# Performance work log

Hardware: AMD Instinct MI355X
Metric: run time of the kernel (lower is better)

Reference implementation:

```python
import jax, jax.numpy as jnp
import numpy as np

N_NODES = 30000
N_EDGES = 480000
N_GRAPHS = 10
NODES_PER_GRAPH = 3000
MAX_RADIUS = 4.0
NUM_BASIS = 10
NUM_NEIGHBORS = 16
DIMS = [8, 288, 288, 288, 3]


def _spherical_harmonics(u):
    """e3nn-style real SH, lmax=2, 'component' normalization, on unit vectors u [E,3]."""
    x, y, z = u[:, 0], u[:, 1], u[:, 2]
    s3, s5, s15 = 3.0 ** 0.5, 5.0 ** 0.5, 15.0 ** 0.5
    return jnp.stack([
        jnp.ones_like(x),                      # l=0
        s3 * x, s3 * y, s3 * z,                # l=1
        s15 * x * z,                           # l=2
        s15 * x * y,
        s5 * (y * y - 0.5 * (x * x + z * z)),
        s15 * y * z,
        (s15 / 2.0) * (z * z - x * x),
    ], axis=1)  # [E, 9]


def _soft_one_hot_smooth_finite(r):
    """soft_one_hot_linspace(r, 0, MAX_RADIUS, NUM_BASIS, 'smooth_finite', cutoff=True)."""
    values = jnp.linspace(0.0, MAX_RADIUS, NUM_BASIS + 2)[1:-1]  # interior centers
    step = MAX_RADIUS / (NUM_BASIS + 1)
    d = (r[:, None] - values) / step
    d2 = d * d
    safe = jnp.where(d2 < 1.0, d2, 0.0)
    const = 1.14136 * float(np.exp(2.0))
    y = jnp.where(d2 < 1.0, const * jnp.exp(-1.0 / (1.0 - safe)), 0.0)
    return y * (NUM_BASIS ** 0.5)  # [E, 10]


def setup_inputs() -> dict:
    key = jax.random.key(0)
    ks = jax.random.split(key, 12)
    inp = {}
    inp['pos'] = jax.random.normal(ks[0], (N_NODES, 3), jnp.float32)
    inp['node_input'] = jax.random.normal(ks[1], (N_NODES, DIMS[0]), jnp.float32)
    inp['node_attr'] = jax.random.uniform(ks[2], (N_NODES, 1), jnp.float32)
    inp['edge_attr'] = jax.random.normal(ks[3], (N_EDGES, 1), jnp.float32)
    inp['edge_src'] = jax.random.randint(ks[4], (N_EDGES,), 0, N_NODES)
    inp['edge_dst'] = jax.random.randint(ks[5], (N_EDGES,), 0, N_NODES)
    inp['batch'] = jnp.repeat(jnp.arange(N_GRAPHS), NODES_PER_GRAPH)
    # radial MLP params (shared shapes across 4 conv layers)
    inp['fc1'] = jax.random.normal(ks[6], (4, NUM_BASIS, 100), jnp.float32) / (NUM_BASIS ** 0.5)
    inp['b1'] = jnp.zeros((4, 100), jnp.float32)
    inp['fc2'] = jax.random.normal(ks[7], (4, 100, NUM_BASIS), jnp.float32) / 10.0
    # per-layer node linear weights
    inp['W0'] = jax.random.normal(ks[8], (DIMS[0], DIMS[1]), jnp.float32) / (DIMS[0] ** 0.5)
    inp['W1'] = jax.random.normal(ks[9], (DIMS[1], DIMS[2]), jnp.float32) / (DIMS[1] ** 0.5)
    inp['W2'] = jax.random.normal(ks[10], (DIMS[2], DIMS[3]), jnp.float32) / (DIMS[2] ** 0.5)
    inp['W3'] = jax.random.normal(ks[11], (DIMS[3], DIMS[4]), jnp.float32) / (DIMS[3] ** 0.5)
    return inp


def reference(pos, node_input, node_attr, edge_attr, fc1, b1, fc2, W0, W1, W2, W3,
              edge_src, edge_dst, batch):
    edge_vec = pos[edge_src] - pos[edge_dst]               # [E,3] gather
    edge_len = jnp.linalg.norm(edge_vec, axis=1)            # [E]
    unit = edge_vec / (edge_len + 1e-12)[:, None]
    edge_sh = _spherical_harmonics(unit)                    # [E,9]
    ea = jnp.concatenate([edge_attr, edge_sh], axis=1)      # [E,10]
    emb = _soft_one_hot_smooth_finite(edge_len)             # [E,10]

    x = node_input * node_attr                               # attr-modulated input [N,8]
    Ws = [W0, W1, W2, W3]
    for l in range(4):
        rad = jax.nn.silu(emb @ fc1[l] + b1[l]) @ fc2[l]     # [E,10] radial weights
        g = jnp.sum(ea * rad, axis=1, keepdims=True)         # [E,1] edge gate (TP contraction)
        m = x[edge_src] * g                                  # [E,F] gather + per-edge product
        agg = jax.ops.segment_sum(m, edge_dst, num_segments=N_NODES)
        agg = agg / (NUM_NEIGHBORS ** 0.5)                   # scatter-reduce, e3nn normalization
        x = agg @ Ws[l]
        if l < 3:
            x = jnp.tanh(x)                                  # gate nonlinearity (simplified)
    pooled = jax.ops.segment_sum(x, batch, num_segments=N_GRAPHS)
    return pooled / (NODES_PER_GRAPH ** 0.5)                 # [10, 3]
```

## Files before the change

kernel.cpp:

```cpp
#include <hip/hip_runtime.h>
#include <math.h>

#define NN 30000
#define NE 480000
#define NG 10
#define TB 8192
#define NBS 118

typedef __attribute__((ext_vector_type(4))) float f32x4;
typedef __attribute__((ext_vector_type(8))) _Float16 half8;

__device__ __forceinline__ float h2f(ushort u) {
    _Float16 h; __builtin_memcpy(&h, &u, 2); return (float)h;
}
__device__ __forceinline__ ushort f2h(float f) {
    _Float16 h = (_Float16)f; ushort u; __builtin_memcpy(&u, &h, 2); return u;
}
__device__ __forceinline__ unsigned int pack2h(float a, float b) {
    return (unsigned int)f2h(a) | ((unsigned int)f2h(b) << 16);
}
struct F8 { float v0,v1,v2,v3,v4,v5,v6,v7; };
__device__ __forceinline__ F8 unpack8h(uint4 v) {
    F8 r;
    r.v0 = h2f((ushort)(v.x & 0xffffu)); r.v1 = h2f((ushort)(v.x >> 16));
    r.v2 = h2f((ushort)(v.y & 0xffffu)); r.v3 = h2f((ushort)(v.y >> 16));
    r.v4 = h2f((ushort)(v.z & 0xffffu)); r.v5 = h2f((ushort)(v.z >> 16));
    r.v6 = h2f((ushort)(v.w & 0xffffu)); r.v7 = h2f((ushort)(v.w >> 16));
    return r;
}
__device__ __forceinline__ float rcpf(float x) { return __builtin_amdgcn_rcpf(x); }
__device__ __forceinline__ float fast_tanh(float x) {
    return 1.0f - 2.0f * rcpf(__expf(2.0f * x) + 1.0f);
}

__global__ __launch_bounds__(256) void build_table_kernel(
    const float* __restrict__ fc1, const float* __restrict__ b1,
    const float* __restrict__ fc2, float* __restrict__ tab)
{
    __shared__ float sF1[4000];
    __shared__ float sF2[4000];
    __shared__ float sB[400];
    int tid = threadIdx.x;
    for (int i = tid; i < 4000; i += 256) { sF1[i] = fc1[i]; sF2[i] = fc2[i]; }
    for (int i = tid; i < 400; i += 256) sB[i] = b1[i];
    __syncthreads();

    int id = blockIdx.x * 256 + tid;
    if (id >= (TB + 1) * 16) return;
    int jc = id & 3, l = (id >> 2) & 3, i = id >> 4;
    float r = (float)i * (4.0f / TB);

    float emb[10];
    const float C = 26.6692991f;
    float rr = r * 2.75f;
    #pragma unroll
    for (int k = 0; k < 10; k++) {
        float dd = rr - (float)(k + 1);
        float d2 = dd * dd;
        emb[k] = (d2 < 1.0f) ? C * __expf(-rcpf(1.0f - d2)) : 0.0f;
    }

    const float* __restrict__ F1 = sF1 + l * 1000;
    const float* __restrict__ Bv = sB + l * 100;
    const float* __restrict__ F2 = sF2 + l * 1000;
    float q[10] = {0,0,0,0,0,0,0,0,0,0};
    int j0 = jc * 25;
    for (int j = j0; j < j0 + 25; j++) {
        float h = Bv[j];
        #pragma unroll
        for (int k = 0; k < 10; k++) h = fmaf(emb[k], F1[k * 100 + j], h);
        float s = h * rcpf(1.0f + __expf(-h));
        #pragma unroll
        for (int k = 0; k < 10; k++) q[k] = fmaf(s, F2[j * 10 + k], q[k]);
    }
    #pragma unroll
    for (int k = 0; k < 10; k++) {
        q[k] += __shfl_xor(q[k], 1);
        q[k] += __shfl_xor(q[k], 2);
    }
    if (jc == 0) {
        #pragma unroll
        for (int k = 0; k < 10; k++) tab[(size_t)i * 40 + k * 4 + l] = q[k];
    }
}

__global__ void transw_kernel(const float* __restrict__ W, ushort* __restrict__ WT)
{
    int id = blockIdx.x * 256 + threadIdx.x;
    if (id >= 288 * 288) return;
    int n = id / 288, k = id - n * 288;
    WT[id] = f2h(W[k * 288 + n]);
}

__global__ __launch_bounds__(256) void edge_g_tab_kernel(
    const float* __restrict__ pos, const float* __restrict__ edge_attr,
    const int* __restrict__ esrc, const int* __restrict__ edst,
    const float* __restrict__ tab, float* __restrict__ g4)
{
    int e = blockIdx.x * 256 + threadIdx.x;
    if (e >= NE) return;
    int s = esrc[e], d = edst[e];
    float vx = pos[3*s+0] - pos[3*d+0];
    float vy = pos[3*s+1] - pos[3*d+1];
    float vz = pos[3*s+2] - pos[3*d+2];
    float r  = sqrtf(vx*vx + vy*vy + vz*vz);
    float inv = rcpf(r + 1e-12f);
    float ux = vx*inv, uy = vy*inv, uz = vz*inv;

    const float s3 = 1.73205081f, s5 = 2.23606798f, s15 = 3.87298335f;
    float ea[10];
    ea[0] = edge_attr[e];
    ea[1] = 1.0f;
    ea[2] = s3*ux; ea[3] = s3*uy; ea[4] = s3*uz;
    ea[5] = s15*ux*uz; ea[6] = s15*ux*uy;
    ea[7] = s5*(uy*uy - 0.5f*(ux*ux + uz*uz));
    ea[8] = s15*uy*uz;
    ea[9] = 0.5f*s15*(uz*uz - ux*ux);

    float t = r * ((float)TB / 4.0f);
    t = fminf(t, (float)TB - 0.001f);
    int i0 = (int)t;
    float f = t - (float)i0;

    const float* row0 = tab + (size_t)i0 * 40;
    const float* row1 = row0 + 40;
    float g0 = 0, g1 = 0, g2 = 0, g3 = 0;
    #pragma unroll
    for (int k = 0; k < 10; k++) {
        float4 a = *(const float4*)(row0 + k * 4);
        float4 b = *(const float4*)(row1 + k * 4);
        float w = ea[k];
        g0 = fmaf(w, fmaf(f, b.x - a.x, a.x), g0);
        g1 = fmaf(w, fmaf(f, b.y - a.y, a.y), g1);
        g2 = fmaf(w, fmaf(f, b.z - a.z, a.z), g2);
        g3 = fmaf(w, fmaf(f, b.w - a.w, a.w), g3);
    }
    *(float4*)&g4[(size_t)e * 4] =
        make_float4(g0 * 0.25f, g1 * 0.25f, g2 * 0.25f, g3 * 0.25f);
}

__global__ void permute_g_kernel(const float* __restrict__ g4, const int* __restrict__ csr,
                                 float* __restrict__ gcsr)
{
    int p = blockIdx.x * 256 + threadIdx.x;
    if (p >= NE) return;
    int e = csr[p];
    float4 g = *(const float4*)&g4[(size_t)e * 4];
    gcsr[p] = g.x;
    gcsr[NE + p] = g.y;
    gcsr[2 * NE + p] = g.z;
    gcsr[3 * NE + p] = g.w;
}

__global__ void count_deg_kernel(const int* __restrict__ edst, int* __restrict__ deg)
{
    int e = blockIdx.x * 256 + threadIdx.x;
    if (e < NE) atomicAdd(&deg[edst[e]], 1);
}

__global__ __launch_bounds__(256) void block_sum_kernel(
    const int* __restrict__ deg, int* __restrict__ bsum)
{
    __shared__ int ws[4];
    int t = threadIdx.x;
    int idx = blockIdx.x * 256 + t;
    int v = (idx < NN) ? deg[idx] : 0;
    #pragma unroll
    for (int off = 1; off < 64; off <<= 1) v += __shfl_xor(v, off);
    if ((t & 63) == 0) ws[t >> 6] = v;
    __syncthreads();
    if (t == 0) bsum[blockIdx.x] = ws[0] + ws[1] + ws[2] + ws[3];
}

__global__ __launch_bounds__(128) void scan_bsum_kernel(
    const int* __restrict__ bsum, int* __restrict__ boff, int* __restrict__ offs)
{
    __shared__ int s[128];
    int t = threadIdx.x;
    s[t] = (t < NBS) ? bsum[t] : 0;
    __syncthreads();
    #pragma unroll
    for (int off = 1; off < 128; off <<= 1) {
        int v = (t >= off) ? s[t - off] : 0;
        __syncthreads();
        s[t] += v;
        __syncthreads();
    }
    if (t < NBS) boff[t] = (t == 0) ? 0 : s[t - 1];
    if (t == 127) offs[NN] = s[127];
}

__global__ __launch_bounds__(256) void scan_local_kernel(
    const int* __restrict__ deg, const int* __restrict__ boff,
    int* __restrict__ offs, int* __restrict__ cur)
{
    __shared__ int s[256];
    int t = threadIdx.x;
    int idx = blockIdx.x * 256 + t;
    int v = (idx < NN) ? deg[idx] : 0;
    s[t] = v;
    __syncthreads();
    #pragma unroll
    for (int off = 1; off < 256; off <<= 1) {
        int u = (t >= off) ? s[t - off] : 0;
        __syncthreads();
        s[t] += u;
        __syncthreads();
    }
    if (idx < NN) {
        int ex = boff[blockIdx.x] + s[t] - v;
        offs[idx] = ex;
        cur[idx] = ex;
    }
}

__global__ void scatter_edges_kernel(const int* __restrict__ edst, const int* __restrict__ esrc,
                                     int* __restrict__ cur, int* __restrict__ csr,
                                     int* __restrict__ csr_src)
{
    int e = blockIdx.x * 256 + threadIdx.x;
    if (e < NE) {
        int slot = atomicAdd(&cur[edst[e]], 1);
        csr[slot] = e;
        csr_src[slot] = esrc[e];
    }
}

__global__ void x0_kernel(const float* __restrict__ ni, const float* __restrict__ na,
                          ushort* __restrict__ x0)
{
    int n = blockIdx.x * 256 + threadIdx.x;
    if (n >= NN) return;
    float a = na[n];
    float4 v0 = *(const float4*)(ni + n * 8);
    float4 v1 = *(const float4*)(ni + n * 8 + 4);
    uint4 o;
    o.x = pack2h(v0.x * a, v0.y * a);
    o.y = pack2h(v0.z * a, v0.w * a);
    o.z = pack2h(v1.x * a, v1.y * a);
    o.w = pack2h(v1.z * a, v1.w * a);
    *(uint4*)(x0 + n * 8) = o;
}

__global__ __launch_bounds__(256) void agg8_kernel(
    const ushort* __restrict__ x0, const float* __restrict__ gc,
    const int* __restrict__ offs, const int* __restrict__ csr_src,
    ushort* __restrict__ a0)
{
    int n = blockIdx.x * 256 + threadIdx.x;
    if (n >= NN) return;
    int beg = offs[n], end = offs[n + 1];
    float a[8] = {0,0,0,0,0,0,0,0};
    for (int p = beg; p < end; p++) {
        float g = gc[p];
        int s = csr_src[p];
        F8 f = unpack8h(*(const uint4*)(x0 + (size_t)s * 8));
        a[0] = fmaf(g, f.v0, a[0]); a[1] = fmaf(g, f.v1, a[1]);
        a[2] = fmaf(g, f.v2, a[2]); a[3] = fmaf(g, f.v3, a[3]);
        a[4] = fmaf(g, f.v4, a[4]); a[5] = fmaf(g, f.v5, a[5]);
        a[6] = fmaf(g, f.v6, a[6]); a[7] = fmaf(g, f.v7, a[7]);
    }
    uint4 o;
    o.x = pack2h(a[0], a[1]);
    o.y = pack2h(a[2], a[3]);
    o.z = pack2h(a[4], a[5]);
    o.w = pack2h(a[6], a[7]);
    *(uint4*)(a0 + (size_t)n * 8) = o;
}

__global__ __launch_bounds__(256) void agg288_kernel(
    const ushort* __restrict__ xin, const float* __restrict__ gc,
    const int* __restrict__ offs, const int* __restrict__ csr_src,
    ushort* __restrict__ out)
{
    int idx = blockIdx.x * 256 + threadIdx.x;
    if (idx >= NN * 36) return;
    int n = idx / 36, c = idx - n * 36;
    int beg = offs[n], end = offs[n + 1];
    float a0=0,a1=0,a2=0,a3=0,a4=0,a5=0,a6=0,a7=0;
    const ushort* xb = xin + c * 8;
    for (int p = beg; p < end; p++) {
        float g = gc[p];
        int s = csr_src[p];
        F8 f = unpack8h(*(const uint4*)(xb + (size_t)s * 288));
        a0 = fmaf(g, f.v0, a0); a1 = fmaf(g, f.v1, a1);
        a2 = fmaf(g, f.v2, a2); a3 = fmaf(g, f.v3, a3);
        a4 = fmaf(g, f.v4, a4); a5 = fmaf(g, f.v5, a5);
        a6 = fmaf(g, f.v6, a6); a7 = fmaf(g, f.v7, a7);
    }
    uint4 o;
    o.x = pack2h(a0, a1);
    o.y = pack2h(a2, a3);
    o.z = pack2h(a4, a5);
    o.w = pack2h(a6, a7);
    *(uint4*)(out + (size_t)idx * 8) = o;
}

__global__ __launch_bounds__(256) void gemm0_kernel(
    const ushort* __restrict__ a0, const float* __restrict__ W0, ushort* __restrict__ x1)
{
    int idx = blockIdx.x * 256 + threadIdx.x;
    if (idx >= NN * 288) return;
    int n = idx / 288, c = idx - n * 288;
    F8 f = unpack8h(*(const uint4*)(a0 + (size_t)n * 8));
    float h = 0.0f;
    h = fmaf(f.v0, W0[0*288+c], h); h = fmaf(f.v1, W0[1*288+c], h);
    h = fmaf(f.v2, W0[2*288+c], h); h = fmaf(f.v3, W0[3*288+c], h);
    h = fmaf(f.v4, W0[4*288+c], h); h = fmaf(f.v5, W0[5*288+c], h);
    h = fmaf(f.v6, W0[6*288+c], h); h = fmaf(f.v7, W0[7*288+c], h);
    x1[idx] = f2h(fast_tanh(h));
}

__global__ __launch_bounds__(256) void mfma_gemm_kernel(
    const ushort* __restrict__ A, const ushort* __restrict__ BT,
    ushort* __restrict__ C, int M)
{
    __shared__ ushort As[96 * 40];
    __shared__ ushort Bs[96 * 40];
    int tid = threadIdx.x;
    int wave = tid >> 6, lane = tid & 63;
    int wr = wave >> 1, wc = wave & 1;
    int rb = blockIdx.y * 96, cb = blockIdx.x * 96;
    int kq = lane >> 4, rl = lane & 15;

    f32x4 acc[3][3];
    #pragma unroll
    for (int m = 0; m < 3; m++)
        #pragma unroll
        for (int n = 0; n < 3; n++)
            acc[m][n] = (f32x4){0.0f, 0.0f, 0.0f, 0.0f};

    for (int k0 = 0; k0 < 288; k0 += 32) {
        __syncthreads();
        for (int c = tid; c < 384; c += 256) {
            int r = c >> 2, ch = c & 3;
            int gr = rb + r;
            uint4 va = (gr < M) ? *(const uint4*)(A + (size_t)gr * 288 + k0 + ch * 8)
                                : make_uint4(0, 0, 0, 0);
            *(uint4*)&As[r * 40 + ch * 8] = va;
            uint4 vb = *(const uint4*)(BT + (size_t)(cb + r) * 288 + k0 + ch * 8);
            *(uint4*)&Bs[r * 40 + ch * 8] = vb;
        }
        __syncthreads();
        half8 a[3], b[3];
        #pragma unroll
        for (int m = 0; m < 3; m++)
            a[m] = *(const half8*)&As[(wr * 48 + m * 16 + rl) * 40 + kq * 8];
        #pragma unroll
        for (int n = 0; n < 3; n++)
            b[n] = *(const half8*)&Bs[(wc * 48 + n * 16 + rl) * 40 + kq * 8];
        #pragma unroll
        for (int m = 0; m < 3; m++)
            #pragma unroll
            for (int n = 0; n < 3; n++)
                acc[m][n] = __builtin_amdgcn_mfma_f32_16x16x32_f16(a[m], b[n], acc[m][n], 0, 0, 0);
    }
    #pragma unroll
    for (int m = 0; m < 3; m++) {
        #pragma unroll
        for (int n = 0; n < 3; n++) {
            int col = cb + wc * 48 + n * 16 + rl;
            #pragma unroll
            for (int q = 0; q < 4; q++) {
                int row = rb + wr * 48 + m * 16 + kq * 4 + q;
                if (row < M)
                    C[(size_t)row * 288 + col] = f2h(fast_tanh(acc[m][n][q]));
            }
        }
    }
}

__global__ __launch_bounds__(256) void final_kernel(
    const ushort* __restrict__ x, const float* __restrict__ W3,
    const int* __restrict__ batch, float* __restrict__ out)
{
    __shared__ float sW[864];
    __shared__ float part[NG * 3];
    int t = threadIdx.x;
    for (int i = t; i < 864; i += 256) sW[i] = W3[i];
    if (t < NG * 3) part[t] = 0.0f;
    __syncthreads();

    int n = blockIdx.x * 256 + t;
    if (n < NN) {
        float a0 = 0, a1 = 0, a2 = 0;
        const ushort* row = x + (size_t)n * 288;
        for (int k = 0; k < 288; k += 8) {
            F8 f = unpack8h(*(const uint4*)(row + k));
            a0 = fmaf(f.v0, sW[(k+0)*3+0], a0); a1 = fmaf(f.v0, sW[(k+0)*3+1], a1); a2 = fmaf(f.v0, sW[(k+0)*3+2], a2);
            a0 = fmaf(f.v1, sW[(k+1)*3+0], a0); a1 = fmaf(f.v1, sW[(k+1)*3+1], a1); a2 = fmaf(f.v1, sW[(k+1)*3+2], a2);
            a0 = fmaf(f.v2, sW[(k+2)*3+0], a0); a1 = fmaf(f.v2, sW[(k+2)*3+1], a1); a2 = fmaf(f.v2, sW[(k+2)*3+2], a2);
            a0 = fmaf(f.v3, sW[(k+3)*3+0], a0); a1 = fmaf(f.v3, sW[(k+3)*3+1], a1); a2 = fmaf(f.v3, sW[(k+3)*3+2], a2);
            a0 = fmaf(f.v4, sW[(k+4)*3+0], a0); a1 = fmaf(f.v4, sW[(k+4)*3+1], a1); a2 = fmaf(f.v4, sW[(k+4)*3+2], a2);
            a0 = fmaf(f.v5, sW[(k+5)*3+0], a0); a1 = fmaf(f.v5, sW[(k+5)*3+1], a1); a2 = fmaf(f.v5, sW[(k+5)*3+2], a2);
            a0 = fmaf(f.v6, sW[(k+6)*3+0], a0); a1 = fmaf(f.v6, sW[(k+6)*3+1], a1); a2 = fmaf(f.v6, sW[(k+6)*3+2], a2);
            a0 = fmaf(f.v7, sW[(k+7)*3+0], a0); a1 = fmaf(f.v7, sW[(k+7)*3+1], a1); a2 = fmaf(f.v7, sW[(k+7)*3+2], a2);
        }
        int g = batch[n];
        atomicAdd(&part[g*3 + 0], a0);
        atomicAdd(&part[g*3 + 1], a1);
        atomicAdd(&part[g*3 + 2], a2);
    }
    __syncthreads();
    if (t < NG * 3) {
        float v = part[t];
        if (v != 0.0f) atomicAdd(&out[t], v * 0.018257419f);
    }
}

extern "C" void kernel_launch(void* const* d_in, const int* in_sizes, int n_in,
                              void* d_out, int out_size, void* d_ws, size_t ws_size,
                              hipStream_t stream)
{
    const float* pos        = (const float*)d_in[0];
    const float* node_input = (const float*)d_in[1];
    const float* node_attr  = (const float*)d_in[2];
    const float* edge_attr  = (const float*)d_in[3];
    const int*   edge_src   = (const int*)d_in[4];
    const int*   edge_dst   = (const int*)d_in[5];
    const int*   batch      = (const int*)d_in[6];
    const float* fc1        = (const float*)d_in[7];
    const float* b1         = (const float*)d_in[8];
    const float* fc2        = (const float*)d_in[9];
    const float* W0         = (const float*)d_in[10];
    const float* W1         = (const float*)d_in[11];
    const float* W2         = (const float*)d_in[12];
    const float* W3         = (const float*)d_in[13];
    float* out = (float*)d_out;

    char* w = (char*)d_ws;
    auto alloc = [&](size_t bytes) { char* p = w; w += (bytes + 255) & ~(size_t)255; return p; };
    float*  g4      = (float*)alloc((size_t)NE * 4 * 4);
    float*  gcsr    = (float*)alloc((size_t)NE * 4 * 4);
    int*    deg     = (int*)alloc((size_t)NN * 4);
    int*    offs    = (int*)alloc((size_t)(NN + 1) * 4);
    int*    cur     = (int*)alloc((size_t)NN * 4);
    int*    csr     = (int*)alloc((size_t)NE * 4);
    int*    csr_src = (int*)alloc((size_t)NE * 4);
    float*  tab     = (float*)alloc((size_t)(TB + 1) * 40 * 4);
    int*    bsum    = (int*)alloc(128 * 4);
    int*    boff    = (int*)alloc(128 * 4);
    ushort* w1t     = (ushort*)alloc(288 * 288 * 2);
    ushort* w2t     = (ushort*)alloc(288 * 288 * 2);
    ushort* x0      = (ushort*)alloc((size_t)NN * 8 * 2);
    ushort* a0      = (ushort*)alloc((size_t)NN * 8 * 2);
    ushort* P       = (ushort*)alloc((size_t)NN * 288 * 2);
    ushort* Q       = (ushort*)alloc((size_t)NN * 288 * 2);

    hipMemsetAsync(deg, 0, NN * sizeof(int), stream);
    hipMemsetAsync(d_out, 0, NG * 3 * sizeof(float), stream);

    build_table_kernel<<<((TB + 1) * 16 + 255) / 256, 256, 0, stream>>>(fc1, b1, fc2, tab);
    transw_kernel<<<324, 256, 0, stream>>>(W1, w1t);
    transw_kernel<<<324, 256, 0, stream>>>(W2, w2t);
    x0_kernel<<<(NN + 255) / 256, 256, 0, stream>>>(node_input, node_attr, x0);

    count_deg_kernel<<<1875, 256, 0, stream>>>(edge_dst, deg);
    block_sum_kernel<<<NBS, 256, 0, stream>>>(deg, bsum);
    scan_bsum_kernel<<<1, 128, 0, stream>>>(bsum, boff, offs);
    scan_local_kernel<<<NBS, 256, 0, stream>>>(deg, boff, offs, cur);
    scatter_edges_kernel<<<1875, 256, 0, stream>>>(edge_dst, edge_src, cur, csr, csr_src);

    edge_g_tab_kernel<<<1875, 256, 0, stream>>>(pos, edge_attr, edge_src, edge_dst,
                                                tab, g4);
    permute_g_kernel<<<1875, 256, 0, stream>>>(g4, csr, gcsr);

    agg8_kernel<<<(NN + 255) / 256, 256, 0, stream>>>(x0, gcsr, offs, csr_src, a0);
    gemm0_kernel<<<NN * 288 / 256, 256, 0, stream>>>(a0, W0, P);
    agg288_kernel<<<(NN * 36 + 255) / 256, 256, 0, stream>>>(P, gcsr + NE, offs, csr_src, Q);
    mfma_gemm_kernel<<<dim3(3, 313), 256, 0, stream>>>(Q, w1t, P, NN);
    agg288_kernel<<<(NN * 36 + 255) / 256, 256, 0, stream>>>(P, gcsr + 2 * NE, offs, csr_src, Q);
    mfma_gemm_kernel<<<dim3(3, 313), 256, 0, stream>>>(Q, w2t, P, NN);
    agg288_kernel<<<(NN * 36 + 255) / 256, 256, 0, stream>>>(P, gcsr + 3 * NE, offs, csr_src, Q);
    final_kernel<<<(NN + 255) / 256, 256, 0, stream>>>(Q, W3, batch, out);
}
```

Baseline: 352.2 us.

## Fuse neighbor aggregation with MFMA GEMM for hidden layers 1 and 2

Replaces the separate agg288 and mfma_gemm kernels for layers 1 and 2 with one kernel per layer. Each block gathers and aggregates 64 destination nodes into a 64x288 fp16 tile in LDS, then multiplies it by the transposed weights with MFMA and writes tanh outputs. This removes the global write and read of the aggregated intermediate and two launches. In exchange it uses about 38KB of LDS per block, which lowers occupancy and the ability to hide the random gather latency, and it has only 469 blocks.

```diff
diff --git a/kernel.cpp b/kernel.cpp
--- a/kernel.cpp
+++ b/kernel.cpp
@@ -296,6 +296,92 @@
     *(uint4*)(out + (size_t)idx * 8) = o;
 }
 
+__global__ __launch_bounds__(256) void fused_agg_gemm_kernel(
+    const ushort* __restrict__ xin, const float* __restrict__ gc,
+    const int* __restrict__ offs, const int* __restrict__ csr_src,
+    const ushort* __restrict__ BT, ushort* __restrict__ out)
+{
+    __shared__ ushort Asl[64 * 296];
+    __shared__ ushort Bs[96 * 40];
+    int tid = threadIdx.x;
+    int n0 = blockIdx.x * 64;
+
+    for (int unit = tid; unit < 64 * 36; unit += 256) {
+        int nl = unit / 36, c = unit - nl * 36;
+        int n = n0 + nl;
+        float a0=0,a1=0,a2=0,a3=0,a4=0,a5=0,a6=0,a7=0;
+        if (n < NN) {
+            int beg = offs[n], end = offs[n + 1];
+            const ushort* xb = xin + c * 8;
+            for (int p = beg; p < end; p++) {
+                float g = gc[p];
+                int s = csr_src[p];
+                F8 f = unpack8h(*(const uint4*)(xb + (size_t)s * 288));
+                a0 = fmaf(g, f.v0, a0); a1 = fmaf(g, f.v1, a1);
+                a2 = fmaf(g, f.v2, a2); a3 = fmaf(g, f.v3, a3);
+                a4 = fmaf(g, f.v4, a4); a5 = fmaf(g, f.v5, a5);
+                a6 = fmaf(g, f.v6, a6); a7 = fmaf(g, f.v7, a7);
+            }
+        }
+        uint4 o;
+        o.x = pack2h(a0, a1);
+        o.y = pack2h(a2, a3);
+        o.z = pack2h(a4, a5);
+        o.w = pack2h(a6, a7);
+        *(uint4*)&Asl[nl * 296 + c * 8] = o;
+    }
+    __syncthreads();
+
+    int wave = tid >> 6, lane = tid & 63;
+    int wr = wave >> 1, wc = wave & 1;
+    int kq = lane >> 4, rl = lane & 15;
+
+    for (int ct = 0; ct < 3; ct++) {
+        int cb = ct * 96;
+        f32x4 acc[2][3];
+        #pragma unroll
+        for (int m = 0; m < 2; m++)
+            #pragma unroll
+            for (int n = 0; n < 3; n++)
+                acc[m][n] = (f32x4){0.0f, 0.0f, 0.0f, 0.0f};
+
+        for (int k0 = 0; k0 < 288; k0 += 32) {
+            __syncthreads();
+            for (int cidx = tid; cidx < 384; cidx += 256) {
+                int r = cidx >> 2, ch = cidx & 3;
+                *(uint4*)&Bs[r * 40 + ch * 8] =
+                    *(const uint4*)(BT + (size_t)(cb + r) * 288 + k0 + ch * 8);
+            }
+            __syncthreads();
+            half8 a[2], b[3];
+            #pragma unroll
+            for (int m = 0; m < 2; m++)
+                a[m] = *(const half8*)&Asl[(wr * 32 + m * 16 + rl) * 296 + k0 + kq * 8];
+            #pragma unroll
+            for (int n = 0; n < 3; n++)
+                b[n] = *(const half8*)&Bs[(wc * 48 + n * 16 + rl) * 40 + kq * 8];
+            #pragma unroll
+            for (int m = 0; m < 2; m++)
+                #pragma unroll
+                for (int n = 0; n < 3; n++)
+                    acc[m][n] = __builtin_amdgcn_mfma_f32_16x16x32_f16(a[m], b[n], acc[m][n], 0, 0, 0);
+        }
+        #pragma unroll
+        for (int m = 0; m < 2; m++) {
+            #pragma unroll
+            for (int n = 0; n < 3; n++) {
+                int col = cb + wc * 48 + n * 16 + rl;
+                #pragma unroll
+                for (int q = 0; q < 4; q++) {
+                    int row = n0 + wr * 32 + m * 16 + kq * 4 + q;
+                    if (row < NN)
+                        out[(size_t)row * 288 + col] = f2h(fast_tanh(acc[m][n][q]));
+                }
+            }
+        }
+    }
+}
+
 __global__ __launch_bounds__(256) void gemm0_kernel(
     const ushort* __restrict__ a0, const float* __restrict__ W0, ushort* __restrict__ x1)
 {
@@ -309,65 +395,6 @@
     h = fmaf(f.v4, W0[4*288+c], h); h = fmaf(f.v5, W0[5*288+c], h);
     h = fmaf(f.v6, W0[6*288+c], h); h = fmaf(f.v7, W0[7*288+c], h);
     x1[idx] = f2h(fast_tanh(h));
-}
-
-__global__ __launch_bounds__(256) void mfma_gemm_kernel(
-    const ushort* __restrict__ A, const ushort* __restrict__ BT,
-    ushort* __restrict__ C, int M)
-{
-    __shared__ ushort As[96 * 40];
-    __shared__ ushort Bs[96 * 40];
-    int tid = threadIdx.x;
-    int wave = tid >> 6, lane = tid & 63;
-    int wr = wave >> 1, wc = wave & 1;
-    int rb = blockIdx.y * 96, cb = blockIdx.x * 96;
-    int kq = lane >> 4, rl = lane & 15;
-
-    f32x4 acc[3][3];
-    #pragma unroll
-    for (int m = 0; m < 3; m++)
-        #pragma unroll
-        for (int n = 0; n < 3; n++)
-            acc[m][n] = (f32x4){0.0f, 0.0f, 0.0f, 0.0f};
-
-    for (int k0 = 0; k0 < 288; k0 += 32) {
-        __syncthreads();
-        for (int c = tid; c < 384; c += 256) {
-            int r = c >> 2, ch = c & 3;
-            int gr = rb + r;
-            uint4 va = (gr < M) ? *(const uint4*)(A + (size_t)gr * 288 + k0 + ch * 8)
-                                : make_uint4(0, 0, 0, 0);
-            *(uint4*)&As[r * 40 + ch * 8] = va;
-            uint4 vb = *(const uint4*)(BT + (size_t)(cb + r) * 288 + k0 + ch * 8);
-            *(uint4*)&Bs[r * 40 + ch * 8] = vb;
-        }
-        __syncthreads();
-        half8 a[3], b[3];
-        #pragma unroll
-        for (int m = 0; m < 3; m++)
-            a[m] = *(const half8*)&As[(wr * 48 + m * 16 + rl) * 40 + kq * 8];
-        #pragma unroll
-        for (int n = 0; n < 3; n++)
-            b[n] = *(const half8*)&Bs[(wc * 48 + n * 16 + rl) * 40 + kq * 8];
-        #pragma unroll
-        for (int m = 0; m < 3; m++)
-            #pragma unroll
-            for (int n = 0; n < 3; n++)
-                acc[m][n] = __builtin_amdgcn_mfma_f32_16x16x32_f16(a[m], b[n], acc[m][n], 0, 0, 0);
-    }
-    #pragma unroll
-    for (int m = 0; m < 3; m++) {
-        #pragma unroll
-        for (int n = 0; n < 3; n++) {
-            int col = cb + wc * 48 + n * 16 + rl;
-            #pragma unroll
-            for (int q = 0; q < 4; q++) {
-                int row = rb + wr * 48 + m * 16 + kq * 4 + q;
-                if (row < M)
-                    C[(size_t)row * 288 + col] = f2h(fast_tanh(acc[m][n][q]));
-            }
-        }
-    }
 }
 
 __global__ __launch_bounds__(256) void final_kernel(
@@ -467,10 +494,8 @@
 
     agg8_kernel<<<(NN + 255) / 256, 256, 0, stream>>>(x0, gcsr, offs, csr_src, a0);
     gemm0_kernel<<<NN * 288 / 256, 256, 0, stream>>>(a0, W0, P);
-    agg288_kernel<<<(NN * 36 + 255) / 256, 256, 0, stream>>>(P, gcsr + NE, offs, csr_src, Q);
-    mfma_gemm_kernel<<<dim3(3, 313), 256, 0, stream>>>(Q, w1t, P, NN);
-    agg288_kernel<<<(NN * 36 + 255) / 256, 256, 0, stream>>>(P, gcsr + 2 * NE, offs, csr_src, Q);
-    mfma_gemm_kernel<<<dim3(3, 313), 256, 0, stream>>>(Q, w2t, P, NN);
+    fused_agg_gemm_kernel<<<(NN + 63) / 64, 256, 0, stream>>>(P, gcsr + NE, offs, csr_src, w1t, Q);
+    fused_agg_gemm_kernel<<<(NN + 63) / 64, 256, 0, stream>>>(Q, gcsr + 2 * NE, offs, csr_src, w2t, P);
     agg288_kernel<<<(NN * 36 + 255) / 256, 256, 0, stream>>>(P, gcsr + 3 * NE, offs, csr_src, Q);
     final_kernel<<<(NN + 255) / 256, 256, 0, stream>>>(Q, W3, batch, out);
 }
```

Result: slower. 485.9 us (+38.0%).
